# Kernel optimization log

Hardware: AMD Instinct MI355X
Metric: run time of the kernel (lower is better)

## Reference

```python
import jax, jax.numpy as jnp
import numpy as np

B, S, D = 4, 4096, 1024
H, EXPAND, DCONV = 8, 2, 4
DI = D * EXPAND           # d_inner = 2048
HD = DI // H              # head_dim = 256
LN_EPS = 1e-5


def setup_inputs() -> dict:
    key = jax.random.key(0)
    ks = jax.random.split(key, 6)
    scale = lambda fan_in: 1.0 / np.sqrt(fan_in)
    return {
        "x": jax.random.normal(ks[0], (B, S, D), dtype=jnp.float32),
        "norm_w": jnp.ones((D,), dtype=jnp.float32),
        "norm_b": jnp.zeros((D,), dtype=jnp.float32),
        "in_proj_w": jax.random.normal(ks[1], (2 * DI, D), dtype=jnp.float32) * scale(D),
        "conv_w": jax.random.normal(ks[2], (DI, 1, DCONV), dtype=jnp.float32) * scale(DCONV),
        "conv_b": jax.random.normal(ks[3], (DI,), dtype=jnp.float32) * 0.02,
        "out_proj_w": jax.random.normal(ks[4], (D, DI), dtype=jnp.float32) * scale(DI),
        "log_alpha": jax.random.uniform(ks[5], (H,), dtype=jnp.float32,
                                        minval=np.log(0.1), maxval=np.log(0.99)),
    }


def reference(x, norm_w, norm_b, in_proj_w, conv_w, conv_b, out_proj_w, log_alpha):
    residual = x
    # LayerNorm
    mu = jnp.mean(x, axis=-1, keepdims=True)
    var = jnp.var(x, axis=-1, keepdims=True)
    xn = (x - mu) * jax.lax.rsqrt(var + LN_EPS) * norm_w + norm_b
    # input projection -> [B, S, 2*DI]
    xz = jnp.einsum("bsd,ed->bse", xn, in_proj_w)
    x_path, gate = xz[..., :DI], xz[..., DI:]
    # causal depthwise conv1d (torch pads d_conv-1 both sides then slices [:S])
    kernel = jnp.transpose(conv_w, (2, 1, 0))  # [DCONV, 1, DI] (WIO)
    x_path = jax.lax.conv_general_dilated(
        x_path, kernel, window_strides=(1,), padding=[(DCONV - 1, 0)],
        dimension_numbers=("NWC", "WIO", "NWC"), feature_group_count=DI,
    ) + conv_b
    # multi-head scalar-decay linear recurrence: y_t = alpha*y_{t-1} + x_t
    xh = x_path.reshape(B, S, H, HD)
    alpha = jax.nn.sigmoid(log_alpha)[:, None]  # [H, 1]

    def step(y, xt):
        y = alpha * y + xt
        return y, y

    y0 = jnp.zeros((B, H, HD), dtype=x.dtype)
    _, ys = jax.lax.scan(step, y0, jnp.transpose(xh, (1, 0, 2, 3)))  # [S, B, H, HD]
    x_path = jnp.transpose(ys, (1, 0, 2, 3)).reshape(B, S, DI)
    # gate + output projection (dropout in eval mode = identity)
    x_path = jax.nn.silu(x_path) * gate
    out = jnp.einsum("bse,de->bsd", x_path, out_proj_w)
    return out + residual
```

## Files before the change

kernel.cpp:

```cpp
#include <hip/hip_runtime.h>
#include <hip/hip_bf16.h>
#include <cstdint>

#define Bb 4
#define Ss 4096
#define Dd 1024
#define Hh 8
#define DI 2048
#define HD 256
#define XZN 4096
#define Mtot 16384
#define NCH 128
#define CHUNK 32

typedef __bf16 bf16_t;
typedef __bf16 bf16x8 __attribute__((ext_vector_type(8)));
typedef __bf16 bf16x4 __attribute__((ext_vector_type(4)));
typedef float f32x4 __attribute__((ext_vector_type(4)));

__device__ __forceinline__ float sigmoidf_(float x) { return 1.f / (1.f + __expf(-x)); }

__device__ __forceinline__ void async_ld16(void* lds, const void* g) {
  __builtin_amdgcn_global_load_lds(
      (const __attribute__((address_space(1))) void*)(uintptr_t)g,
      (__attribute__((address_space(3))) void*)(uint32_t)(uintptr_t)lds,
      16, 0, 0);
}

__global__ __launch_bounds__(256) void cvt_kernel(const float* __restrict__ s,
                                                  bf16_t* __restrict__ d) {
  const int i = blockIdx.x * 256 + threadIdx.x;
  const float4 v = ((const float4*)s)[i];
  bf16_t* o = d + 4 * (size_t)i;
  o[0] = (bf16_t)v.x; o[1] = (bf16_t)v.y; o[2] = (bf16_t)v.z; o[3] = (bf16_t)v.w;
}

__global__ __launch_bounds__(256) void ln_kernel(const float* __restrict__ x,
                                                 const float* __restrict__ w,
                                                 const float* __restrict__ b,
                                                 bf16_t* __restrict__ xn) {
  __shared__ float red[8];
  const int row = blockIdx.x;
  const float4 v = ((const float4*)(x + (size_t)row * Dd))[threadIdx.x];
  float s  = v.x + v.y + v.z + v.w;
  float s2 = v.x * v.x + v.y * v.y + v.z * v.z + v.w * v.w;
  #pragma unroll
  for (int off = 32; off; off >>= 1) { s += __shfl_down(s, off); s2 += __shfl_down(s2, off); }
  const int wave = threadIdx.x >> 6, lane = threadIdx.x & 63;
  if (lane == 0) { red[wave * 2] = s; red[wave * 2 + 1] = s2; }
  __syncthreads();
  if (threadIdx.x == 0) {
    float S = 0.f, S2 = 0.f;
    for (int i = 0; i < 4; ++i) { S += red[i * 2]; S2 += red[i * 2 + 1]; }
    red[0] = S; red[1] = S2;
  }
  __syncthreads();
  const float mean = red[0] * (1.f / Dd);
  const float var  = red[1] * (1.f / Dd) - mean * mean;
  const float rstd = rsqrtf(var + 1e-5f);
  const float4 wv = ((const float4*)w)[threadIdx.x];
  const float4 bv = ((const float4*)b)[threadIdx.x];
  bf16_t* o = xn + (size_t)row * Dd + threadIdx.x * 4;
  o[0] = (bf16_t)((v.x - mean) * rstd * wv.x + bv.x);
  o[1] = (bf16_t)((v.y - mean) * rstd * wv.y + bv.y);
  o[2] = (bf16_t)((v.z - mean) * rstd * wv.z + bv.z);
  o[3] = (bf16_t)((v.w - mean) * rstd * wv.w + bv.w);
}

template <int ADD_RES>
__global__ __launch_bounds__(512, 2) void gemm256(const bf16_t* __restrict__ A,
                                                  const bf16_t* __restrict__ Bw,
                                                  void* __restrict__ Cv,
                                                  const float* __restrict__ res,
                                                  int M, int N, int K) {
  __shared__ __align__(16) char LDS[131072];
  const int tid = threadIdx.x;
  const int wave = tid >> 6, lane = tid & 63;
  const int wm = wave >> 2, wn = wave & 3;

  const int nbx = gridDim.x;
  const int nwg = nbx * gridDim.y;
  const int bid0 = blockIdx.y * nbx + blockIdx.x;
  const int cpx = nwg >> 3;
  const int bid = (bid0 & 7) * cpx + (bid0 >> 3);
  const int bm = bid / nbx, bn = bid % nbx;

  f32x4 acc[8][4];
  #pragma unroll
  for (int i = 0; i < 8; ++i)
    #pragma unroll
    for (int j = 0; j < 4; ++j) acc[i][j] = (f32x4){0.f, 0.f, 0.f, 0.f};

  const int scg = (lane & 3) ^ ((lane >> 3) & 3);
  const bf16_t* Ag = A  + (size_t)(bm * 256 + wave * 16 + (lane >> 2)) * K + scg * 8;
  const bf16_t* Bg = Bw + (size_t)(bn * 256 + wave * 16 + (lane >> 2)) * K + scg * 8;
  const size_t rowK128 = (size_t)128 * K;
  char* const LDSw = LDS + wave * 1024;

  const int fr = lane & 15, fq = lane >> 4;
  int aoff[8], boff[4];
  #pragma unroll
  for (int mt = 0; mt < 8; ++mt) {
    const int row = wm * 128 + mt * 16 + fr;
    aoff[mt] = row * 64 + ((fq ^ ((row >> 1) & 3)) << 4);
  }
  #pragma unroll
  for (int nt = 0; nt < 4; ++nt) {
    const int row = wn * 64 + nt * 16 + fr;
    boff[nt] = row * 64 + ((fq ^ ((row >> 1) & 3)) << 4);
  }

  const int NT = K >> 6;

#define STG(u, mat, ks) do {                                              \
    char* d_ = LDSw + ((u) & 1) * 65536 + (mat) * 32768 + (ks) * 16384;   \
    const bf16_t* s_ = (mat) ? Bg : Ag;                                   \
    const int ko_ = (u) * 64 + (ks) * 32;                                 \
    async_ld16(d_,        s_ + ko_);                                      \
    async_ld16(d_ + 8192, s_ + rowK128 + ko_);                            \
  } while (0)

#define RDA(DST, bufb, ks, g) do {                                        \
    _Pragma("unroll")                                                     \
    for (int i_ = 0; i_ < 4; ++i_)                                        \
      DST[i_] = *(const bf16x8*)(LDS + (bufb) * 65536 + (ks) * 16384 + aoff[(g) * 4 + i_]); \
  } while (0)

#define RDB(DST, bufb, ks) do {                                           \
    _Pragma("unroll")                                                     \
    for (int i_ = 0; i_ < 4; ++i_)                                        \
      DST[i_] = *(const bf16x8*)(LDS + (bufb) * 65536 + 32768 + (ks) * 16384 + boff[i_]); \
  } while (0)

#define MM(AF, BF, g) do {                                                \
    __builtin_amdgcn_s_setprio(1);                                        \
    _Pragma("unroll")                                                     \
    for (int m_ = 0; m_ < 4; ++m_)                                        \
      _Pragma("unroll")                                                   \
      for (int n_ = 0; n_ < 4; ++n_)                                      \
        acc[(g) * 4 + m_][n_] = __builtin_amdgcn_mfma_f32_16x16x32_bf16(  \
            AF[m_], BF[n_], acc[(g) * 4 + m_][n_], 0, 0, 0);              \
    __builtin_amdgcn_s_setprio(0);                                        \
  } while (0)

#define LGKM0 do { asm volatile("s_waitcnt lgkmcnt(0)" ::: "memory");     \
    __builtin_amdgcn_sched_barrier(0); } while (0)
#define VMB4 do { asm volatile("s_waitcnt vmcnt(4)" ::: "memory");        \
    __builtin_amdgcn_s_barrier(); } while (0)
#define VMB0 do { asm volatile("s_waitcnt vmcnt(0)" ::: "memory");        \
    __builtin_amdgcn_s_barrier(); } while (0)

  STG(0, 0, 0); STG(0, 1, 0); STG(0, 0, 1); STG(0, 1, 1);
  bf16x8 af[4], ag[4], bfk[4];

  for (int t = 0; t < NT - 1; ++t) {
    const int cb = t & 1;
    VMB4;
    RDB(bfk, cb, 0); RDA(af, cb, 0, 0);
    STG(t + 1, 0, 0);
    LGKM0; MM(af, bfk, 0);
    RDA(ag, cb, 0, 1);
    STG(t + 1, 1, 0);
    LGKM0; MM(ag, bfk, 1);
    VMB4;
    RDB(bfk, cb, 1); RDA(af, cb, 1, 0);
    STG(t + 1, 0, 1);
    LGKM0; MM(af, bfk, 0);
    RDA(ag, cb, 1, 1);
    STG(t + 1, 1, 1);
    LGKM0; MM(ag, bfk, 1);
  }
  {
    const int cb = (NT - 1) & 1;
    VMB4;
    RDB(bfk, cb, 0); RDA(af, cb, 0, 0);
    LGKM0; MM(af, bfk, 0);
    RDA(ag, cb, 0, 1);
    LGKM0; MM(ag, bfk, 1);
    VMB0;
    RDB(bfk, cb, 1); RDA(af, cb, 1, 0);
    LGKM0; MM(af, bfk, 0);
    RDA(ag, cb, 1, 1);
    LGKM0; MM(ag, bfk, 1);
  }

#undef STG
#undef RDA
#undef RDB
#undef MM
#undef LGKM0
#undef VMB4
#undef VMB0

  const int m0 = bm * 256 + wm * 128 + fq * 4;
  const int n0 = bn * 256 + wn * 64 + fr;
  #pragma unroll
  for (int mt = 0; mt < 8; ++mt)
    #pragma unroll
    for (int nt = 0; nt < 4; ++nt)
      #pragma unroll
      for (int r = 0; r < 4; ++r) {
        const size_t m = (size_t)(m0 + mt * 16 + r);
        const size_t n = (size_t)(n0 + nt * 16);
        if (ADD_RES)
          ((float*)Cv)[m * N + n] = acc[mt][nt][r] + res[m * N + n];
        else
          ((bf16_t*)Cv)[m * N + n] = (bf16_t)acc[mt][nt][r];
      }
}

__global__ __launch_bounds__(256) void scanA_kernel(const bf16_t* __restrict__ xz,
                                                    const float* __restrict__ conv_w,
                                                    const float* __restrict__ conv_b,
                                                    const float* __restrict__ log_alpha,
                                                    float* __restrict__ carry) {
  const int half  = blockIdx.x & 1;
  const int chunk = (blockIdx.x >> 1) & (NCH - 1);
  const int b     = blockIdx.x >> 8;
  const int ch    = half * 1024 + threadIdx.x * 4;
  const float alpha = sigmoidf_(log_alpha[ch >> 8]);
  float w[4][4], bias[4];
  #pragma unroll
  for (int j = 0; j < 4; ++j) {
    const float4 cw = ((const float4*)conv_w)[ch + j];
    w[j][0] = cw.x; w[j][1] = cw.y; w[j][2] = cw.z; w[j][3] = cw.w;
    bias[j] = conv_b[ch + j];
  }
  const int s0 = chunk * CHUNK;
  const size_t base = ((size_t)b * Ss + s0) * XZN + ch;
  float x3[4] = {0,0,0,0}, x2[4] = {0,0,0,0}, x1[4] = {0,0,0,0}, y[4] = {0,0,0,0};
  if (chunk > 0) {
    const bf16x4 v3 = *(const bf16x4*)(xz + base - 3 * (size_t)XZN);
    const bf16x4 v2 = *(const bf16x4*)(xz + base - 2 * (size_t)XZN);
    const bf16x4 v1 = *(const bf16x4*)(xz + base - 1 * (size_t)XZN);
    #pragma unroll
    for (int j = 0; j < 4; ++j) { x3[j] = (float)v3[j]; x2[j] = (float)v2[j]; x1[j] = (float)v1[j]; }
  }
  #pragma unroll 4
  for (int t = 0; t < CHUNK; ++t) {
    const bf16x4 v = *(const bf16x4*)(xz + base + (size_t)t * XZN);
    #pragma unroll
    for (int j = 0; j < 4; ++j) {
      const float xc = (float)v[j];
      const float cv = bias[j] + w[j][0] * x3[j] + w[j][1] * x2[j] + w[j][2] * x1[j] + w[j][3] * xc;
      x3[j] = x2[j]; x2[j] = x1[j]; x1[j] = xc;
      y[j] = fmaf(alpha, y[j], cv);
    }
  }
  *(float4*)(carry + ((size_t)b * NCH + chunk) * DI + ch) =
      make_float4(y[0], y[1], y[2], y[3]);
}

__global__ __launch_bounds__(256) void scanB_kernel(const float* __restrict__ carry,
                                                    float* __restrict__ carryin,
                                                    const float* __restrict__ log_alpha) {
  __shared__ float S[8][32];
  const int b   = blockIdx.x >> 6;
  const int chg = blockIdx.x & 63;
  const int cg  = threadIdx.x >> 5;
  const int chl = threadIdx.x & 31;
  const int ch  = chg * 32 + chl;
  const float alpha = sigmoidf_(log_alpha[ch >> 8]);
  const float lal  = log2f(alpha);
  const float aL   = exp2f((float)CHUNK * lal);
  const float aL16 = exp2f((float)(CHUNK * 16) * lal);
  const size_t base = ((size_t)b * NCH + cg * 16) * DI + ch;
  float v[16];
  #pragma unroll
  for (int i = 0; i < 16; ++i) v[i] = carry[base + (size_t)i * DI];
  float Sl = v[0];
  #pragma unroll
  for (int i = 1; i < 16; ++i) Sl = fmaf(aL, Sl, v[i]);
  S[cg][chl] = Sl;
  __syncthreads();
  float P = 0.f;
  for (int h = 0; h < cg; ++h) P = fmaf(aL16, P, S[h][chl]);
  #pragma unroll
  for (int i = 0; i < 16; ++i) {
    carryin[base + (size_t)i * DI] = P;
    P = fmaf(aL, P, v[i]);
  }
}

__global__ __launch_bounds__(256) void scanC_kernel(const bf16_t* __restrict__ xz,
                                                    const float* __restrict__ conv_w,
                                                    const float* __restrict__ conv_b,
                                                    const float* __restrict__ log_alpha,
                                                    const float* __restrict__ carryin,
                                                    bf16_t* __restrict__ act) {
  const int half  = blockIdx.x & 1;
  const int chunk = (blockIdx.x >> 1) & (NCH - 1);
  const int b     = blockIdx.x >> 8;
  const int ch    = half * 1024 + threadIdx.x * 4;
  const float alpha = sigmoidf_(log_alpha[ch >> 8]);
  float w[4][4], bias[4];
  #pragma unroll
  for (int j = 0; j < 4; ++j) {
    const float4 cw = ((const float4*)conv_w)[ch + j];
    w[j][0] = cw.x; w[j][1] = cw.y; w[j][2] = cw.z; w[j][3] = cw.w;
    bias[j] = conv_b[ch + j];
  }
  const int s0 = chunk * CHUNK;
  const size_t base = ((size_t)b * Ss + s0) * XZN + ch;
  float x3[4] = {0,0,0,0}, x2[4] = {0,0,0,0}, x1[4] = {0,0,0,0}, y[4];
  const float4 cin = *(const float4*)(carryin + ((size_t)b * NCH + chunk) * DI + ch);
  y[0] = cin.x; y[1] = cin.y; y[2] = cin.z; y[3] = cin.w;
  if (chunk > 0) {
    const bf16x4 v3 = *(const bf16x4*)(xz + base - 3 * (size_t)XZN);
    const bf16x4 v2 = *(const bf16x4*)(xz + base - 2 * (size_t)XZN);
    const bf16x4 v1 = *(const bf16x4*)(xz + base - 1 * (size_t)XZN);
    #pragma unroll
    for (int j = 0; j < 4; ++j) { x3[j] = (float)v3[j]; x2[j] = (float)v2[j]; x1[j] = (float)v1[j]; }
  }
  const size_t abase = ((size_t)b * Ss + s0) * DI + ch;
  #pragma unroll 4
  for (int t = 0; t < CHUNK; ++t) {
    const bf16x4 v = *(const bf16x4*)(xz + base + (size_t)t * XZN);
    const bf16x4 gv = *(const bf16x4*)(xz + base + (size_t)t * XZN + DI);
    bf16x4 ov;
    #pragma unroll
    for (int j = 0; j < 4; ++j) {
      const float xc = (float)v[j];
      const float cv = bias[j] + w[j][0] * x3[j] + w[j][1] * x2[j] + w[j][2] * x1[j] + w[j][3] * xc;
      x3[j] = x2[j]; x2[j] = x1[j]; x1[j] = xc;
      y[j] = fmaf(alpha, y[j], cv);
      const float o = y[j] * (1.f / (1.f + __expf(-y[j]))) * (float)gv[j];
      ov[j] = (bf16_t)o;
    }
    *(bf16x4*)(act + abase + (size_t)t * DI) = ov;
  }
}

extern "C" void kernel_launch(void* const* d_in, const int* in_sizes, int n_in,
                              void* d_out, int out_size, void* d_ws, size_t ws_size,
                              hipStream_t stream) {
  const float* x          = (const float*)d_in[0];
  const float* norm_w     = (const float*)d_in[1];
  const float* norm_b     = (const float*)d_in[2];
  const float* in_proj_w  = (const float*)d_in[3];
  const float* conv_w     = (const float*)d_in[4];
  const float* conv_b     = (const float*)d_in[5];
  const float* out_proj_w = (const float*)d_in[6];
  const float* log_alpha  = (const float*)d_in[7];
  float* out = (float*)d_out;

  char* ws = (char*)d_ws;
  bf16_t* xn     = (bf16_t*)(ws);
  bf16_t* w_in   = (bf16_t*)(ws + 33554432);
  bf16_t* w_out  = (bf16_t*)(ws + 41943040);
  bf16_t* xz     = (bf16_t*)(ws + 46137344);
  bf16_t* act    = (bf16_t*)(ws + 180355072);
  float*  carry   = (float*)(ws);
  float*  carryin = (float*)(ws + 4194304);

  cvt_kernel<<<4096, 256, 0, stream>>>(in_proj_w, w_in);
  cvt_kernel<<<2048, 256, 0, stream>>>(out_proj_w, w_out);
  ln_kernel<<<Mtot, 256, 0, stream>>>(x, norm_w, norm_b, xn);

  dim3 g1(XZN / 256, Mtot / 256);
  gemm256<0><<<g1, 512, 0, stream>>>(xn, w_in, xz, nullptr, Mtot, XZN, Dd);

  scanA_kernel<<<Bb * NCH * 2, 256, 0, stream>>>(xz, conv_w, conv_b, log_alpha, carry);
  scanB_kernel<<<Bb * 64, 256, 0, stream>>>(carry, carryin, log_alpha);
  scanC_kernel<<<Bb * NCH * 2, 256, 0, stream>>>(xz, conv_w, conv_b, log_alpha, carryin, act);

  dim3 g2(Dd / 256, Mtot / 256);
  gemm256<1><<<g2, 512, 0, stream>>>(act, w_out, out, x, Mtot, Dd, DI);
}
```

Baseline: 392.2 us.

## Templatize GEMM tiles, use 128x128 tiles for out-proj, widen scan vectors, merge weight casts

The GEMM becomes a template over wave grid and per-wave tile counts. The output projection now uses 128x128 tiles with 256 threads, giving 1024 workgroups instead of 256 so the CUs are filled better, at the cost of less operand reuse per tile. The s_setprio hints are removed. The scan kernels now process 8 channels per thread with 16-byte loads and stores, using half as many blocks, and the two weight-conversion launches are merged into one.

```diff
diff --git a/kernel.cpp b/kernel.cpp
--- a/kernel.cpp
+++ b/kernel.cpp
@@ -27,11 +27,17 @@
       16, 0, 0);
 }
 
-__global__ __launch_bounds__(256) void cvt_kernel(const float* __restrict__ s,
-                                                  bf16_t* __restrict__ d) {
-  const int i = blockIdx.x * 256 + threadIdx.x;
+__global__ __launch_bounds__(256) void cvt2_kernel(const float* __restrict__ a,
+                                                   bf16_t* __restrict__ da,
+                                                   const float* __restrict__ b,
+                                                   bf16_t* __restrict__ db) {
+  const int na = (2 * DI * Dd) / 4;
+  int i = blockIdx.x * 256 + threadIdx.x;
+  const float* s;
+  bf16_t* o;
+  if (i < na) { s = a; o = da + 4 * (size_t)i; }
+  else        { i -= na; s = b; o = db + 4 * (size_t)i; }
   const float4 v = ((const float4*)s)[i];
-  bf16_t* o = d + 4 * (size_t)i;
   o[0] = (bf16_t)v.x; o[1] = (bf16_t)v.y; o[2] = (bf16_t)v.z; o[3] = (bf16_t)v.w;
 }
 
@@ -67,16 +73,23 @@
   o[3] = (bf16_t)((v.w - mean) * rstd * wv.w + bv.w);
 }
 
-template <int ADD_RES>
-__global__ __launch_bounds__(512, 2) void gemm256(const bf16_t* __restrict__ A,
-                                                  const bf16_t* __restrict__ Bw,
-                                                  void* __restrict__ Cv,
-                                                  const float* __restrict__ res,
-                                                  int M, int N, int K) {
-  __shared__ __align__(16) char LDS[131072];
+template <int ADD_RES, int WM, int WN, int MT, int NTT>
+__global__ __launch_bounds__(WM * WN * 64, 2) void gemm_t(const bf16_t* __restrict__ A,
+                                                          const bf16_t* __restrict__ Bw,
+                                                          void* __restrict__ Cv,
+                                                          const float* __restrict__ res,
+                                                          int M, int N, int K) {
+  constexpr int WAVES = WM * WN;
+  constexpr int BM = WM * MT * 16;
+  constexpr int BN = WN * NTT * 16;
+  static_assert(BM == BN, "square tiles only");
+  constexpr int RSZ  = BM * 64;
+  constexpr int BUFB = 4 * RSZ;
+  constexpr int HALFROWS = WAVES * 16;
+  __shared__ __align__(16) char LDS[2 * BUFB];
   const int tid = threadIdx.x;
   const int wave = tid >> 6, lane = tid & 63;
-  const int wm = wave >> 2, wn = wave & 3;
+  const int wm = wave / WN, wn = wave % WN;
 
   const int nbx = gridDim.x;
   const int nwg = nbx * gridDim.y;
@@ -85,62 +98,62 @@
   const int bid = (bid0 & 7) * cpx + (bid0 >> 3);
   const int bm = bid / nbx, bn = bid % nbx;
 
-  f32x4 acc[8][4];
-  #pragma unroll
-  for (int i = 0; i < 8; ++i)
-    #pragma unroll
-    for (int j = 0; j < 4; ++j) acc[i][j] = (f32x4){0.f, 0.f, 0.f, 0.f};
-
   const int scg = (lane & 3) ^ ((lane >> 3) & 3);
-  const bf16_t* Ag = A  + (size_t)(bm * 256 + wave * 16 + (lane >> 2)) * K + scg * 8;
-  const bf16_t* Bg = Bw + (size_t)(bn * 256 + wave * 16 + (lane >> 2)) * K + scg * 8;
-  const size_t rowK128 = (size_t)128 * K;
+  const bf16_t* Ag = A  + (size_t)(bm * BM + wave * 16 + (lane >> 2)) * K + scg * 8;
+  const bf16_t* Bg = Bw + (size_t)(bn * BN + wave * 16 + (lane >> 2)) * K + scg * 8;
+  const size_t rowHK = (size_t)HALFROWS * K;
   char* const LDSw = LDS + wave * 1024;
 
-  const int fr = lane & 15, fq = lane >> 4;
-  int aoff[8], boff[4];
-  #pragma unroll
-  for (int mt = 0; mt < 8; ++mt) {
-    const int row = wm * 128 + mt * 16 + fr;
-    aoff[mt] = row * 64 + ((fq ^ ((row >> 1) & 3)) << 4);
-  }
-  #pragma unroll
-  for (int nt = 0; nt < 4; ++nt) {
-    const int row = wn * 64 + nt * 16 + fr;
-    boff[nt] = row * 64 + ((fq ^ ((row >> 1) & 3)) << 4);
-  }
-
-  const int NT = K >> 6;
-
 #define STG(u, mat, ks) do {                                              \
-    char* d_ = LDSw + ((u) & 1) * 65536 + (mat) * 32768 + (ks) * 16384;   \
+    char* d_ = LDSw + ((u) & 1) * BUFB + (mat) * 2 * RSZ + (ks) * RSZ;    \
     const bf16_t* s_ = (mat) ? Bg : Ag;                                   \
     const int ko_ = (u) * 64 + (ks) * 32;                                 \
-    async_ld16(d_,        s_ + ko_);                                      \
-    async_ld16(d_ + 8192, s_ + rowK128 + ko_);                            \
-  } while (0)
+    async_ld16(d_,           s_ + ko_);                                   \
+    async_ld16(d_ + RSZ / 2, s_ + rowHK + ko_);                           \
+  } while (0)
+
+  const int NT = K >> 6;
+
+  STG(0, 0, 0); STG(0, 1, 0); STG(0, 0, 1); STG(0, 1, 1);
+
+  f32x4 acc[MT][NTT];
+  #pragma unroll
+  for (int i = 0; i < MT; ++i)
+    #pragma unroll
+    for (int j = 0; j < NTT; ++j) acc[i][j] = (f32x4){0.f, 0.f, 0.f, 0.f};
+
+  const int fr = lane & 15, fq = lane >> 4;
+  int aoff[MT], boff[NTT];
+  #pragma unroll
+  for (int mt = 0; mt < MT; ++mt) {
+    const int row = wm * MT * 16 + mt * 16 + fr;
+    aoff[mt] = row * 64 + ((fq ^ ((row >> 1) & 3)) << 4);
+  }
+  #pragma unroll
+  for (int nt = 0; nt < NTT; ++nt) {
+    const int row = wn * NTT * 16 + nt * 16 + fr;
+    boff[nt] = row * 64 + ((fq ^ ((row >> 1) & 3)) << 4);
+  }
 
 #define RDA(DST, bufb, ks, g) do {                                        \
     _Pragma("unroll")                                                     \
     for (int i_ = 0; i_ < 4; ++i_)                                        \
-      DST[i_] = *(const bf16x8*)(LDS + (bufb) * 65536 + (ks) * 16384 + aoff[(g) * 4 + i_]); \
+      DST[i_] = *(const bf16x8*)(LDS + (bufb) * BUFB + (ks) * RSZ + aoff[(g) * 4 + i_]); \
   } while (0)
 
 #define RDB(DST, bufb, ks) do {                                           \
     _Pragma("unroll")                                                     \
-    for (int i_ = 0; i_ < 4; ++i_)                                        \
-      DST[i_] = *(const bf16x8*)(LDS + (bufb) * 65536 + 32768 + (ks) * 16384 + boff[i_]); \
-  } while (0)
-
-#define MM(AF, BF, g) do {                                                \
-    __builtin_amdgcn_s_setprio(1);                                        \
+    for (int i_ = 0; i_ < NTT; ++i_)                                      \
+      DST[i_] = *(const bf16x8*)(LDS + (bufb) * BUFB + 2 * RSZ + (ks) * RSZ + boff[i_]); \
+  } while (0)
+
+#define MMx(AF, BF, g) do {                                               \
     _Pragma("unroll")                                                     \
     for (int m_ = 0; m_ < 4; ++m_)                                        \
       _Pragma("unroll")                                                   \
-      for (int n_ = 0; n_ < 4; ++n_)                                      \
+      for (int n_ = 0; n_ < NTT; ++n_)                                    \
         acc[(g) * 4 + m_][n_] = __builtin_amdgcn_mfma_f32_16x16x32_bf16(  \
             AF[m_], BF[n_], acc[(g) * 4 + m_][n_], 0, 0, 0);              \
-    __builtin_amdgcn_s_setprio(0);                                        \
   } while (0)
 
 #define LGKM0 do { asm volatile("s_waitcnt lgkmcnt(0)" ::: "memory");     \
@@ -150,54 +163,49 @@
 #define VMB0 do { asm volatile("s_waitcnt vmcnt(0)" ::: "memory");        \
     __builtin_amdgcn_s_barrier(); } while (0)
 
-  STG(0, 0, 0); STG(0, 1, 0); STG(0, 0, 1); STG(0, 1, 1);
-  bf16x8 af[4], ag[4], bfk[4];
+#define KS_PHASE(t_, cb_, ks_, FULL) do {                                 \
+    RDB(bq, cb_, ks_); RDA(aq, cb_, ks_, 0);                              \
+    if (FULL) STG((t_) + 1, 0, ks_);                                      \
+    if constexpr (MT == 8) {                                              \
+      LGKM0; MMx(aq, bq, 0);                                              \
+      RDA(aq2, cb_, ks_, 1);                                              \
+      if (FULL) STG((t_) + 1, 1, ks_);                                    \
+      LGKM0; MMx(aq2, bq, 1);                                             \
+    } else {                                                              \
+      if (FULL) STG((t_) + 1, 1, ks_);                                    \
+      LGKM0; MMx(aq, bq, 0);                                              \
+    }                                                                     \
+  } while (0)
+
+  bf16x8 aq[4], aq2[4], bq[NTT];
+  (void)aq2;
 
   for (int t = 0; t < NT - 1; ++t) {
     const int cb = t & 1;
-    VMB4;
-    RDB(bfk, cb, 0); RDA(af, cb, 0, 0);
-    STG(t + 1, 0, 0);
-    LGKM0; MM(af, bfk, 0);
-    RDA(ag, cb, 0, 1);
-    STG(t + 1, 1, 0);
-    LGKM0; MM(ag, bfk, 1);
-    VMB4;
-    RDB(bfk, cb, 1); RDA(af, cb, 1, 0);
-    STG(t + 1, 0, 1);
-    LGKM0; MM(af, bfk, 0);
-    RDA(ag, cb, 1, 1);
-    STG(t + 1, 1, 1);
-    LGKM0; MM(ag, bfk, 1);
+    VMB4; KS_PHASE(t, cb, 0, 1);
+    VMB4; KS_PHASE(t, cb, 1, 1);
   }
   {
     const int cb = (NT - 1) & 1;
-    VMB4;
-    RDB(bfk, cb, 0); RDA(af, cb, 0, 0);
-    LGKM0; MM(af, bfk, 0);
-    RDA(ag, cb, 0, 1);
-    LGKM0; MM(ag, bfk, 1);
-    VMB0;
-    RDB(bfk, cb, 1); RDA(af, cb, 1, 0);
-    LGKM0; MM(af, bfk, 0);
-    RDA(ag, cb, 1, 1);
-    LGKM0; MM(ag, bfk, 1);
+    VMB4; KS_PHASE(NT - 1, cb, 0, 0);
+    VMB0; KS_PHASE(NT - 1, cb, 1, 0);
   }
 
 #undef STG
 #undef RDA
 #undef RDB
-#undef MM
+#undef MMx
 #undef LGKM0
 #undef VMB4
 #undef VMB0
-
-  const int m0 = bm * 256 + wm * 128 + fq * 4;
-  const int n0 = bn * 256 + wn * 64 + fr;
-  #pragma unroll
-  for (int mt = 0; mt < 8; ++mt)
-    #pragma unroll
-    for (int nt = 0; nt < 4; ++nt)
+#undef KS_PHASE
+
+  const int m0 = bm * BM + wm * MT * 16 + fq * 4;
+  const int n0 = bn * BN + wn * NTT * 16 + fr;
+  #pragma unroll
+  for (int mt = 0; mt < MT; ++mt)
+    #pragma unroll
+    for (int nt = 0; nt < NTT; ++nt)
       #pragma unroll
       for (int r = 0; r < 4; ++r) {
         const size_t m = (size_t)(m0 + mt * 16 + r);
@@ -214,41 +222,43 @@
                                                     const float* __restrict__ conv_b,
                                                     const float* __restrict__ log_alpha,
                                                     float* __restrict__ carry) {
-  const int half  = blockIdx.x & 1;
-  const int chunk = (blockIdx.x >> 1) & (NCH - 1);
-  const int b     = blockIdx.x >> 8;
-  const int ch    = half * 1024 + threadIdx.x * 4;
+  const int chunk = blockIdx.x & (NCH - 1);
+  const int b     = blockIdx.x >> 7;
+  const int ch    = threadIdx.x * 8;
   const float alpha = sigmoidf_(log_alpha[ch >> 8]);
-  float w[4][4], bias[4];
-  #pragma unroll
-  for (int j = 0; j < 4; ++j) {
+  float w[8][4], bias[8];
+  #pragma unroll
+  for (int j = 0; j < 8; ++j) {
     const float4 cw = ((const float4*)conv_w)[ch + j];
     w[j][0] = cw.x; w[j][1] = cw.y; w[j][2] = cw.z; w[j][3] = cw.w;
     bias[j] = conv_b[ch + j];
   }
   const int s0 = chunk * CHUNK;
   const size_t base = ((size_t)b * Ss + s0) * XZN + ch;
-  float x3[4] = {0,0,0,0}, x2[4] = {0,0,0,0}, x1[4] = {0,0,0,0}, y[4] = {0,0,0,0};
+  float x3[8], x2[8], x1[8], y[8];
+  #pragma unroll
+  for (int j = 0; j < 8; ++j) { x3[j] = x2[j] = x1[j] = y[j] = 0.f; }
   if (chunk > 0) {
-    const bf16x4 v3 = *(const bf16x4*)(xz + base - 3 * (size_t)XZN);
-    const bf16x4 v2 = *(const bf16x4*)(xz + base - 2 * (size_t)XZN);
-    const bf16x4 v1 = *(const bf16x4*)(xz + base - 1 * (size_t)XZN);
-    #pragma unroll
-    for (int j = 0; j < 4; ++j) { x3[j] = (float)v3[j]; x2[j] = (float)v2[j]; x1[j] = (float)v1[j]; }
-  }
-  #pragma unroll 4
+    const bf16x8 v3 = *(const bf16x8*)(xz + base - 3 * (size_t)XZN);
+    const bf16x8 v2 = *(const bf16x8*)(xz + base - 2 * (size_t)XZN);
+    const bf16x8 v1 = *(const bf16x8*)(xz + base - 1 * (size_t)XZN);
+    #pragma unroll
+    for (int j = 0; j < 8; ++j) { x3[j] = (float)v3[j]; x2[j] = (float)v2[j]; x1[j] = (float)v1[j]; }
+  }
+  #pragma unroll 2
   for (int t = 0; t < CHUNK; ++t) {
-    const bf16x4 v = *(const bf16x4*)(xz + base + (size_t)t * XZN);
-    #pragma unroll
-    for (int j = 0; j < 4; ++j) {
+    const bf16x8 v = *(const bf16x8*)(xz + base + (size_t)t * XZN);
+    #pragma unroll
+    for (int j = 0; j < 8; ++j) {
       const float xc = (float)v[j];
       const float cv = bias[j] + w[j][0] * x3[j] + w[j][1] * x2[j] + w[j][2] * x1[j] + w[j][3] * xc;
       x3[j] = x2[j]; x2[j] = x1[j]; x1[j] = xc;
       y[j] = fmaf(alpha, y[j], cv);
     }
   }
-  *(float4*)(carry + ((size_t)b * NCH + chunk) * DI + ch) =
-      make_float4(y[0], y[1], y[2], y[3]);
+  float* cp = carry + ((size_t)b * NCH + chunk) * DI + ch;
+  *(float4*)cp       = make_float4(y[0], y[1], y[2], y[3]);
+  *(float4*)(cp + 4) = make_float4(y[4], y[5], y[6], y[7]);
 }
 
 __global__ __launch_bounds__(256) void scanB_kernel(const float* __restrict__ carry,
@@ -288,38 +298,42 @@
                                                     const float* __restrict__ log_alpha,
                                                     const float* __restrict__ carryin,
                                                     bf16_t* __restrict__ act) {
-  const int half  = blockIdx.x & 1;
-  const int chunk = (blockIdx.x >> 1) & (NCH - 1);
-  const int b     = blockIdx.x >> 8;
-  const int ch    = half * 1024 + threadIdx.x * 4;
+  const int chunk = blockIdx.x & (NCH - 1);
+  const int b     = blockIdx.x >> 7;
+  const int ch    = threadIdx.x * 8;
   const float alpha = sigmoidf_(log_alpha[ch >> 8]);
-  float w[4][4], bias[4];
-  #pragma unroll
-  for (int j = 0; j < 4; ++j) {
+  float w[8][4], bias[8];
+  #pragma unroll
+  for (int j = 0; j < 8; ++j) {
     const float4 cw = ((const float4*)conv_w)[ch + j];
     w[j][0] = cw.x; w[j][1] = cw.y; w[j][2] = cw.z; w[j][3] = cw.w;
     bias[j] = conv_b[ch + j];
   }
   const int s0 = chunk * CHUNK;
   const size_t base = ((size_t)b * Ss + s0) * XZN + ch;
-  float x3[4] = {0,0,0,0}, x2[4] = {0,0,0,0}, x1[4] = {0,0,0,0}, y[4];
-  const float4 cin = *(const float4*)(carryin + ((size_t)b * NCH + chunk) * DI + ch);
-  y[0] = cin.x; y[1] = cin.y; y[2] = cin.z; y[3] = cin.w;
+  float x3[8], x2[8], x1[8], y[8];
+  const float* cp = carryin + ((size_t)b * NCH + chunk) * DI + ch;
+  const float4 ci0 = *(const float4*)cp;
+  const float4 ci1 = *(const float4*)(cp + 4);
+  y[0] = ci0.x; y[1] = ci0.y; y[2] = ci0.z; y[3] = ci0.w;
+  y[4] = ci1.x; y[5] = ci1.y; y[6] = ci1.z; y[7] = ci1.w;
+  #pragma unroll
+  for (int j = 0; j < 8; ++j) { x3[j] = x2[j] = x1[j] = 0.f; }
   if (chunk > 0) {
-    const bf16x4 v3 = *(const bf16x4*)(xz + base - 3 * (size_t)XZN);
-    const bf16x4 v2 = *(const bf16x4*)(xz + base - 2 * (size_t)XZN);
-    const bf16x4 v1 = *(const bf16x4*)(xz + base - 1 * (size_t)XZN);
-    #pragma unroll
-    for (int j = 0; j < 4; ++j) { x3[j] = (float)v3[j]; x2[j] = (float)v2[j]; x1[j] = (float)v1[j]; }
+    const bf16x8 v3 = *(const bf16x8*)(xz + base - 3 * (size_t)XZN);
+    const bf16x8 v2 = *(const bf16x8*)(xz + base - 2 * (size_t)XZN);
+    const bf16x8 v1 = *(const bf16x8*)(xz + base - 1 * (size_t)XZN);
+    #pragma unroll
+    for (int j = 0; j < 8; ++j) { x3[j] = (float)v3[j]; x2[j] = (float)v2[j]; x1[j] = (float)v1[j]; }
   }
   const size_t abase = ((size_t)b * Ss + s0) * DI + ch;
-  #pragma unroll 4
+  #pragma unroll 2
   for (int t = 0; t < CHUNK; ++t) {
-    const bf16x4 v = *(const bf16x4*)(xz + base + (size_t)t * XZN);
-    const bf16x4 gv = *(const bf16x4*)(xz + base + (size_t)t * XZN + DI);
-    bf16x4 ov;
-    #pragma unroll
-    for (int j = 0; j < 4; ++j) {
+    const bf16x8 v  = *(const bf16x8*)(xz + base + (size_t)t * XZN);
+    const bf16x8 gv = *(const bf16x8*)(xz + base + (size_t)t * XZN + DI);
+    bf16x8 ov;
+    #pragma unroll
+    for (int j = 0; j < 8; ++j) {
       const float xc = (float)v[j];
       const float cv = bias[j] + w[j][0] * x3[j] + w[j][1] * x2[j] + w[j][2] * x1[j] + w[j][3] * xc;
       x3[j] = x2[j]; x2[j] = x1[j]; x1[j] = xc;
@@ -327,7 +341,7 @@
       const float o = y[j] * (1.f / (1.f + __expf(-y[j]))) * (float)gv[j];
       ov[j] = (bf16_t)o;
     }
-    *(bf16x4*)(act + abase + (size_t)t * DI) = ov;
+    *(bf16x8*)(act + abase + (size_t)t * DI) = ov;
   }
 }
 
@@ -353,17 +367,16 @@
   float*  carry   = (float*)(ws);
   float*  carryin = (float*)(ws + 4194304);
 
-  cvt_kernel<<<4096, 256, 0, stream>>>(in_proj_w, w_in);
-  cvt_kernel<<<2048, 256, 0, stream>>>(out_proj_w, w_out);
+  cvt2_kernel<<<6144, 256, 0, stream>>>(in_proj_w, w_in, out_proj_w, w_out);
   ln_kernel<<<Mtot, 256, 0, stream>>>(x, norm_w, norm_b, xn);
 
   dim3 g1(XZN / 256, Mtot / 256);
-  gemm256<0><<<g1, 512, 0, stream>>>(xn, w_in, xz, nullptr, Mtot, XZN, Dd);
-
-  scanA_kernel<<<Bb * NCH * 2, 256, 0, stream>>>(xz, conv_w, conv_b, log_alpha, carry);
+  gemm_t<0, 2, 4, 8, 4><<<g1, 512, 0, stream>>>(xn, w_in, xz, nullptr, Mtot, XZN, Dd);
+
+  scanA_kernel<<<Bb * NCH, 256, 0, stream>>>(xz, conv_w, conv_b, log_alpha, carry);
   scanB_kernel<<<Bb * 64, 256, 0, stream>>>(carry, carryin, log_alpha);
-  scanC_kernel<<<Bb * NCH * 2, 256, 0, stream>>>(xz, conv_w, conv_b, log_alpha, carryin, act);
-
-  dim3 g2(Dd / 256, Mtot / 256);
-  gemm256<1><<<g2, 512, 0, stream>>>(act, w_out, out, x, Mtot, Dd, DI);
-}
+  scanC_kernel<<<Bb * NCH, 256, 0, stream>>>(xz, conv_w, conv_b, log_alpha, carryin, act);
+
+  dim3 g2(Dd / 128, Mtot / 128);
+  gemm_t<1, 2, 2, 4, 4><<<g2, 256, 0, stream>>>(act, w_out, out, x, Mtot, Dd, DI);
+}
```

Result: slower. 434.0 us (+10.6%).
